# Kernel tuning notes

Hardware: AMD Instinct MI355X
Metric: run time of the kernel (lower is better)

The kernel has to match this reference:

```python
import jax, jax.numpy as jnp
import numpy as np

Lx, Ly, D, P = 4, 5, 4, 2
DEPTH = 5
TAU = 0.1
N = Lx * Ly
B = 64


def setup_inputs() -> dict:
    key = jax.random.key(0)
    k1, k2, k3 = jax.random.split(key, 3)
    # PEPS site tensors: [Lx, Ly, phys, up, down, left, right]; boundary bonds sliced to dim 1 at use.
    peps = jax.random.normal(k1, (Lx, Ly, P, D, D, D, D), dtype=jnp.float32) * 0.5
    # Two-site Trotter gate: expm(-tau * h) for a random symmetric two-body term h (4x4).
    h = jax.random.normal(k2, (4, 4), dtype=jnp.float32)
    h = 0.5 * (h + h.T)
    w, v = jnp.linalg.eigh(h)
    gate = (v * jnp.exp(-TAU * w)) @ v.T  # [4,4]
    x = jax.random.randint(k3, (B, N), 0, 2, dtype=jnp.int32)
    return {"x": x, "peps": peps, "gate": gate}


def _slice_boundary(site, i, j):
    # site: [p, u, d, l, r]; open boundary -> bond dim 1 on lattice edges
    if i == 0:
        site = site[:, :1]
    if i == Lx - 1:
        site = site[:, :, :1]
    if j == 0:
        site = site[:, :, :, :1]
    if j == Ly - 1:
        site = site[..., :1]
    return site


def _peps_statevector(peps):
    # Exact contraction of the open-boundary PEPS to the full 2^N statevector.
    rows = []
    for i in range(Lx):
        T = jnp.ones((1, 1, 1, 1), dtype=peps.dtype)  # [Pphys, Uup, Ddown, l]
        for j in range(Ly):
            s = _slice_boundary(peps[i, j], i, j)
            T = jnp.einsum('PUDl,pudlr->PpUuDdr', T, s)
            Pn, p, U, u, Dn, d, r = T.shape
            T = T.reshape(Pn * p, U * u, Dn * d, r)
        rows.append(T[..., 0])  # [2^Ly, up_bonds, down_bonds]
    S = jnp.ones((1, 1), dtype=peps.dtype)  # [Pphys, down_bonds]
    for row in rows:
        S = jnp.einsum('PU,QUD->PQD', S, row)
        a, b, c = S.shape
        S = S.reshape(a * b, c)
    return S[:, 0]  # [2^N]


def _apply_gate(psi, g, a, b):
    # g: [2,2,2,2] = gate[o1,o2,i1,i2]; psi: (2,)*N
    out = jnp.tensordot(g, psi, axes=([2, 3], [a, b]))
    return jnp.moveaxis(out, (0, 1), (a, b))


def _bonds():
    horiz = [((i, j), (i, j + 1)) for i in range(Lx) for j in range(Ly - 1)]
    vert = [((i, j), (i + 1, j)) for i in range(Lx - 1) for j in range(Ly)]
    return horiz + vert


def reference(x, peps, gate):
    psi = _peps_statevector(peps).reshape((2,) * N)
    g = gate.reshape(2, 2, 2, 2)
    bonds = _bonds()
    for _ in range(DEPTH):
        for (i1, j1), (i2, j2) in bonds:
            psi = _apply_gate(psi, g, i1 * Ly + j1, i2 * Ly + j2)
    psi = psi.reshape(-1)
    pw = 2 ** jnp.arange(N - 1, -1, -1, dtype=jnp.int32)
    idx = (x * pw).sum(axis=1)
    return psi[idx]  # [B] amplitudes
```

## Files before the change

### kernel.cpp

```cpp
#include <hip/hip_runtime.h>


#define PAD(i) ((i) + (((i) >> 4) << 2))
#define PIDX(i,j,p,u,d,l,r) (((((((i)*5+(j))*2+(p))*4+(u))*4+(d))*4+(l))*4+(r))

static constexpr int COL0  = 0;
static constexpr int COL1  = 4096;
static constexpr int COL2  = COL1 + 1048576;
static constexpr int COL3  = COL2 + 1048576;
static constexpr int COL4  = COL3 + 1048576;
static constexpr int M01TO = COL4 + 4096;
static constexpr int M34TO = M01TO + 65536;
static constexpr int T12TO = M34TO + 65536;
static constexpr int PSIO  = T12TO + 1048576;

__global__ __launch_bounds__(256) void k_build_cols(const float* __restrict__ peps,
                                                    float* __restrict__ ws) {
  __shared__ float p01[4096], p23[4096];
  int bid = blockIdx.x, t = threadIdx.x;
  if (bid < 384) {
    int col = 1 + (bid >> 7);
    int part = bid & 127;
#pragma unroll
    for (int k = 0; k < 16; ++k) {
      int e = k * 256 + t;
      int r12 = e & 15, l12 = (e >> 4) & 15, d2 = (e >> 8) & 3, p = e >> 10;
      int l1 = l12 >> 2, l2 = l12 & 3, r1 = r12 >> 2, r2 = r12 & 3;
      float s01 = 0.f, s23 = 0.f;
#pragma unroll
      for (int d = 0; d < 4; ++d) {
        s01 += peps[PIDX(0, col, (p >> 1), 0, d, l1, r1)] *
               peps[PIDX(1, col, (p & 1), d, d2, l2, r2)];
        s23 += peps[PIDX(2, col, (p >> 1), d2, d, l1, r1)] *
               peps[PIDX(3, col, (p & 1), d, 0, l2, r2)];
      }
      p01[e] = s01;
      p23[e] = s23;
    }
    __syncthreads();
    const int coloffs[3] = {COL1, COL2, COL3};
    float* out = ws + coloffs[col - 1];
#pragma unroll
    for (int k = 0; k < 8; ++k) {
      int eq = part * 8192 + (k * 256 + t) * 4;
      int r34b = eq & 15;
      int r12 = (eq >> 4) & 15, l34 = (eq >> 8) & 15, l12 = (eq >> 12) & 15;
      int p = eq >> 16;
      int pa = p >> 2, pb = p & 3;
      float4 acc = {0.f, 0.f, 0.f, 0.f};
#pragma unroll
      for (int d2 = 0; d2 < 4; ++d2) {
        float a01 = p01[((((pa * 4 + d2) << 4) | l12) << 4) | r12];
        const float4 b4 =
            *(const float4*)&p23[((((pb * 4 + d2) << 4) | l34) << 4) | r34b];
        acc.x += a01 * b4.x;
        acc.y += a01 * b4.y;
        acc.z += a01 * b4.z;
        acc.w += a01 * b4.w;
      }
      *(float4*)&out[eq] = acc;
    }
  } else {
    int col = (bid == 384) ? 0 : 4;
    const int lsh = (col == 0) ? 0 : 2;
    const int rsh = (col == 4) ? 0 : 2;
    const int ldim = 1 << lsh, rdim = 1 << rsh;
    const int LLB = 2 * lsh, RRB = 2 * rsh;
    const int LL = 1 << LLB, RR = 1 << RRB;
    int n12 = (LL * RR) << 4;
    for (int e = t; e < n12; e += 256) {
      int r12 = e & (RR - 1);
      int l12 = (e >> RRB) & (LL - 1);
      int d2 = (e >> (RRB + LLB)) & 3;
      int p = e >> (RRB + LLB + 2);
      int l1 = l12 >> lsh, l2 = l12 & (ldim - 1);
      int r1 = r12 >> rsh, r2 = r12 & (rdim - 1);
      float s01 = 0.f, s23 = 0.f;
      for (int d = 0; d < 4; ++d) {
        s01 += peps[PIDX(0, col, (p >> 1), 0, d, l1, r1)] *
               peps[PIDX(1, col, (p & 1), d, d2, l2, r2)];
        s23 += peps[PIDX(2, col, (p >> 1), d2, d, l1, r1)] *
               peps[PIDX(3, col, (p & 1), d, 0, l2, r2)];
      }
      p01[e] = s01;
      p23[e] = s23;
    }
    __syncthreads();
    const int LB = 2 * LLB, RB = 2 * RRB;
    int total = 16 << (LB + RB);
    float* out = ws + ((col == 0) ? COL0 : COL4);
    for (int e = t; e < total; e += 256) {
      int r = e & ((1 << RB) - 1);
      int l = (e >> RB) & ((1 << LB) - 1);
      int p = e >> (RB + LB);
      int r34 = r & (RR - 1), r12 = r >> RRB;
      int l34 = l & (LL - 1), l12 = l >> LLB;
      int pa = p >> 2, pb = p & 3;
      float s = 0.f;
      for (int d2 = 0; d2 < 4; ++d2) {
        s += p01[((((pa * 4 + d2) << LLB) | l12) << RRB) | r12] *
             p23[((((pb * 4 + d2) << LLB) | l34) << RRB) | r34];
      }
      out[e] = s;
    }
  }
}

__global__ __launch_bounds__(256) void k_small(const float* __restrict__ ws,
                                               float* __restrict__ m01,
                                               float* __restrict__ m34t) {
  __shared__ float c3buf[4112], c4buf[4112];
  int t = threadIdx.x;
  if (blockIdx.x < 64) {
    int c1 = blockIdx.x >> 2, q = blockIdx.x & 3;
    int r2l = t & 63, c0g = t >> 6;
    int R2 = q * 64 + r2l;
    const float* col0 = ws + COL0;
    const float* col1 = ws + COL1;
    float a0 = 0.f, a1 = 0.f, a2 = 0.f, a3 = 0.f;
    for (int R1 = 0; R1 < 256; ++R1) {
      float bv = col1[(c1 * 256 + R1) * 256 + R2];
      a0 += col0[(c0g * 4 + 0) * 256 + R1] * bv;
      a1 += col0[(c0g * 4 + 1) * 256 + R1] * bv;
      a2 += col0[(c0g * 4 + 2) * 256 + R1] * bv;
      a3 += col0[(c0g * 4 + 3) * 256 + R1] * bv;
    }
    m01[((c0g * 4 + 0) * 16 + c1) * 256 + R2] = a0;
    m01[((c0g * 4 + 1) * 16 + c1) * 256 + R2] = a1;
    m01[((c0g * 4 + 2) * 16 + c1) * 256 + R2] = a2;
    m01[((c0g * 4 + 3) * 16 + c1) * 256 + R2] = a3;
  } else {
    int L3 = blockIdx.x - 64;
    const float* col3 = ws + COL3;
    const float* col4 = ws + COL4;
    for (int e = t; e < 4096; e += 256) {
      c4buf[(e >> 8) * 257 + (e & 255)] = col4[e];
      c3buf[(e >> 8) * 257 + (e & 255)] =
          col3[(e >> 8) * 65536 + L3 * 256 + (e & 255)];
    }
    __syncthreads();
    int c3 = t >> 4, c4 = t & 15;
    float acc = 0.f;
    for (int B = 0; B < 256; ++B)
      acc += c3buf[c3 * 257 + B] * c4buf[c4 * 257 + B];
    m34t[L3 * 256 + t] = acc;
  }
}

__global__ __launch_bounds__(256) void k_t012(const float* __restrict__ m01,
                                              const float* __restrict__ col2,
                                              float* __restrict__ t012) {
  __shared__ float A[4096];
  int t = threadIdx.x;
  int c2 = blockIdx.x & 15, tg = blockIdx.x >> 4;
#pragma unroll
  for (int k = 0; k < 4; ++k)
    *(float4*)&A[(k * 256 + t) * 4] =
        *(const float4*)&m01[tg * 4096 + (k * 256 + t) * 4];
  __syncthreads();
  float acc[16] = {};
  for (int R2 = 0; R2 < 256; R2 += 4) {
    float b0 = col2[c2 * 65536 + (R2 + 0) * 256 + t];
    float b1 = col2[c2 * 65536 + (R2 + 1) * 256 + t];
    float b2 = col2[c2 * 65536 + (R2 + 2) * 256 + t];
    float b3 = col2[c2 * 65536 + (R2 + 3) * 256 + t];
#pragma unroll
    for (int i = 0; i < 16; ++i) {
      float4 a4 = *(const float4*)&A[i * 256 + R2];
      acc[i] += a4.x * b0 + a4.y * b1 + a4.z * b2 + a4.w * b3;
    }
  }
#pragma unroll
  for (int i = 0; i < 16; ++i)
    t012[c2 * 65536 + (tg * 16 + i) * 256 + t] = acc[i];
}

__global__ __launch_bounds__(256) void k_psi0(const float* __restrict__ t012,
                                              const float* __restrict__ m34t,
                                              float* __restrict__ psi) {
  __shared__ float A[4096];
  __shared__ float S[4112];
  int t = threadIdx.x;
  int tg = blockIdx.x;
#pragma unroll
  for (int i = 0; i < 16; ++i)
    A[i * 256 + t] = t012[i * 65536 + tg * 256 + t];
  __syncthreads();
  float acc[16] = {};
  for (int L3 = 0; L3 < 256; L3 += 4) {
    float b0 = m34t[(L3 + 0) * 256 + t];
    float b1 = m34t[(L3 + 1) * 256 + t];
    float b2 = m34t[(L3 + 2) * 256 + t];
    float b3 = m34t[(L3 + 3) * 256 + t];
#pragma unroll
    for (int i = 0; i < 16; ++i) {
      float4 a4 = *(const float4*)&A[i * 256 + L3];
      acc[i] += a4.x * b0 + a4.y * b1 + a4.z * b2 + a4.w * b3;
    }
  }
#pragma unroll
  for (int i = 0; i < 16; ++i) S[i * 257 + t] = acc[i];
  __syncthreads();
  int c3 = t >> 4, c2 = t & 15;
  int base = c3 * 65536 + (tg >> 4) * 256 + (tg & 15) * 16 + c2;
#pragma unroll
  for (int v = 0; v < 16; ++v)
    psi[base + v * 4096] = S[c2 * 257 + c3 * 16 + v];
}

template <int NB, int HI, int LO>
__device__ __forceinline__ void gate2(float* x, const float* __restrict__ g) {
  constexpr int H = 1 << HI, L = 1 << LO, N = 1 << NB;
#pragma unroll
  for (int o = 0; o < N; ++o) {
    if (o & (H | L)) continue;
    float v0 = x[o], v1 = x[o + L], v2 = x[o + H], v3 = x[o + H + L];
    x[o]         = g[0]  * v0 + g[1]  * v1 + g[2]  * v2 + g[3]  * v3;
    x[o + L]     = g[4]  * v0 + g[5]  * v1 + g[6]  * v2 + g[7]  * v3;
    x[o + H]     = g[8]  * v0 + g[9]  * v1 + g[10] * v2 + g[11] * v3;
    x[o + H + L] = g[12] * v0 + g[13] * v1 + g[14] * v2 + g[15] * v3;
  }
}

template <int ST>
__device__ __forceinline__ void vxf(float* s, const float* __restrict__ g, int b) {
  float x[16];
#pragma unroll
  for (int m = 0; m < 16; ++m) x[m] = s[PAD(b + m * ST)];
  gate2<4, 3, 2>(x, g);
  gate2<4, 2, 1>(x, g);
  gate2<4, 1, 0>(x, g);
#pragma unroll
  for (int m = 0; m < 16; ++m) s[PAD(b + m * ST)] = x[m];
}

template <int B2, int B1, int B0>
__device__ __forceinline__ void bondpair(float* s, const float* __restrict__ g,
                                         int t) {
  constexpr int MASK = (1 << B2) | (1 << B1) | (1 << B0);
  int b = 0, rem = t;
#pragma unroll
  for (int p = 0; p < 12; ++p) {
    if (!((MASK >> p) & 1)) {
      b |= (rem & 1) << p;
      rem >>= 1;
    }
  }
  float x[8];
#pragma unroll
  for (int m = 0; m < 8; ++m) {
    int off = ((m >> 2) & 1) * (1 << B2) + ((m >> 1) & 1) * (1 << B1) +
              (m & 1) * (1 << B0);
    x[m] = s[PAD(b + off)];
  }
  gate2<3, 2, 1>(x, g);
  gate2<3, 1, 0>(x, g);
#pragma unroll
  for (int m = 0; m < 8; ++m) {
    int off = ((m >> 2) & 1) * (1 << B2) + ((m >> 1) & 1) * (1 << B1) +
              (m & 1) * (1 << B0);
    s[PAD(b + off)] = x[m];
  }
}

__global__ __launch_bounds__(512) void k_P1(float* __restrict__ psi,
                                            const float* __restrict__ gate) {
  __shared__ float s[5120];
  float g[16];
#pragma unroll
  for (int i = 0; i < 16; ++i) g[i] = gate[i];
  int t = threadIdx.x;
  int o = blockIdx.x;
#pragma unroll
  for (int i = 0; i < 2; ++i) {
    int f = (i * 512 + t) * 4;
    *(float4*)(s + PAD(f)) = *(const float4*)(psi + o * 4096 + f);
  }
  __syncthreads();
  bondpair<8, 4, 0>(s, g, t);
  __syncthreads();
  bondpair<9, 5, 1>(s, g, t);
  __syncthreads();
  bondpair<10, 6, 2>(s, g, t);
  __syncthreads();
  bondpair<11, 7, 3>(s, g, t);
  __syncthreads();
  if (t < 256) vxf<256>(s, g, t);
  __syncthreads();
  if (t < 256) vxf<16>(s, g, ((t >> 4) << 8) | (t & 15));
  __syncthreads();
#pragma unroll
  for (int i = 0; i < 2; ++i) {
    int f = (i * 512 + t) * 4;
    *(float4*)(psi + o * 4096 + f) = *(const float4*)(s + PAD(f));
  }
}

template <bool LAST>
__global__ __launch_bounds__(512) void k_P2(float* __restrict__ psi,
                                            const float* __restrict__ gate,
                                            const int* __restrict__ x,
                                            float* __restrict__ out) {
  __shared__ float s[5120];
  float g[16];
#pragma unroll
  for (int i = 0; i < 16; ++i) g[i] = gate[i];
  int t = threadIdx.x;
  int o = blockIdx.x;
#pragma unroll
  for (int i = 0; i < 2; ++i) {
    int f = (i * 512 + t) * 4;
    int addr = (f >> 8) * 65536 + ((f >> 4) & 15) * 4096 + o * 16 + (f & 15);
    *(float4*)(s + PAD(f)) = *(const float4*)(psi + addr);
  }
  __syncthreads();
  bondpair<0, 8, 4>(s, g, t);
  __syncthreads();
  bondpair<1, 9, 5>(s, g, t);
  __syncthreads();
  bondpair<2, 10, 6>(s, g, t);
  __syncthreads();
  bondpair<3, 11, 7>(s, g, t);
  __syncthreads();
  if (t < 256) vxf<1>(s, g, t * 16);
  __syncthreads();
  if (t < 256) vxf<256>(s, g, t);
  __syncthreads();
  if (t < 256) vxf<16>(s, g, ((t >> 4) << 8) | (t & 15));
  __syncthreads();
  if (LAST) {
    if (t < 64) {
      int idx = 0;
#pragma unroll
      for (int q = 0; q < 20; ++q) {
        int i = q / 5, j = q % 5;
        int pos = (j == 0) ? (11 - i)
                 : (j == 1) ? (7 - i)
                 : (j == 2) ? (3 - i)
                 : (j == 3) ? (19 - i)
                            : (15 - i);
        idx |= x[t * 20 + q] << pos;
      }
      if (((idx >> 4) & 255) == o) {
        int local = ((idx >> 16) & 15) * 256 + ((idx >> 12) & 15) * 16 +
                    (idx & 15);
        out[t] = s[PAD(local)];
      }
    }
  } else {
#pragma unroll
    for (int i = 0; i < 2; ++i) {
      int f = (i * 512 + t) * 4;
      int addr = (f >> 8) * 65536 + ((f >> 4) & 15) * 4096 + o * 16 + (f & 15);
      *(float4*)(psi + addr) = *(const float4*)(s + PAD(f));
    }
  }
}

extern "C" void kernel_launch(void* const* d_in, const int* in_sizes, int n_in,
                              void* d_out, int out_size, void* d_ws, size_t ws_size,
                              hipStream_t stream) {
  const int* x = (const int*)d_in[0];
  const float* peps = (const float*)d_in[1];
  const float* gate = (const float*)d_in[2];
  float* ws = (float*)d_ws;
  float* psi = ws + PSIO;
  float* out = (float*)d_out;

  k_build_cols<<<386, 256, 0, stream>>>(peps, ws);
  k_small<<<320, 256, 0, stream>>>(ws, ws + M01TO, ws + M34TO);
  k_t012<<<256, 256, 0, stream>>>(ws + M01TO, ws + COL2, ws + T12TO);
  k_psi0<<<256, 256, 0, stream>>>(ws + T12TO, ws + M34TO, psi);

  for (int it = 0; it < 5; ++it) {
    k_P1<<<256, 512, 0, stream>>>(psi, gate);
    if (it < 4)
      k_P2<false><<<256, 512, 0, stream>>>(psi, gate, x, out);
    else
      k_P2<true><<<256, 512, 0, stream>>>(psi, gate, x, out);
  }
}
```

Measured before the change: 214.6 us.

## Remap gate passes to wave-local index sets, replacing block barriers with wave syncs

Reassigns the thread-to-amplitude mapping in the shared-memory gate passes so that consecutive bond-pair and vxf stages touch index subsets owned by a single wavefront. Several block-wide __syncthreads are replaced with a wave-local LDS wait plus wave barrier. This cuts block-level barrier stalls inside the per-tile gate sequence. Correctness depends on the new mappings keeping each dependent pair of stages inside one wave, and the new addressing may change LDS bank-conflict patterns.

```diff
diff --git a/kernel.cpp b/kernel.cpp
--- a/kernel.cpp
+++ b/kernel.cpp
@@ -3,6 +3,8 @@
 
 #define PAD(i) ((i) + (((i) >> 4) << 2))
 #define PIDX(i,j,p,u,d,l,r) (((((((i)*5+(j))*2+(p))*4+(u))*4+(d))*4+(l))*4+(r))
+#define WSYNC() do { asm volatile("s_waitcnt lgkmcnt(0)" ::: "memory"); \
+                     __builtin_amdgcn_wave_barrier(); } while (0)
 
 static constexpr int COL0  = 0;
 static constexpr int COL1  = 4096;
@@ -235,17 +237,8 @@
 }
 
 template <int B2, int B1, int B0>
-__device__ __forceinline__ void bondpair(float* s, const float* __restrict__ g,
-                                         int t) {
-  constexpr int MASK = (1 << B2) | (1 << B1) | (1 << B0);
-  int b = 0, rem = t;
-#pragma unroll
-  for (int p = 0; p < 12; ++p) {
-    if (!((MASK >> p) & 1)) {
-      b |= (rem & 1) << p;
-      rem >>= 1;
-    }
-  }
+__device__ __forceinline__ void bp_at(float* s, const float* __restrict__ g,
+                                      int b) {
   float x[8];
 #pragma unroll
   for (int m = 0; m < 8; ++m) {
@@ -263,6 +256,27 @@
   }
 }
 
+__device__ __forceinline__ int shA(int w, int l) {
+  return ((w >> 2) & 1) * 2048 + ((w >> 1) & 1) * 1024 + (w & 1) * 128 +
+         ((l >> 5) & 1) * 64 + ((l >> 4) & 1) * 8 + ((l >> 3) & 1) * 4;
+}
+__device__ __forceinline__ int shB(int w, int l) {
+  return ((w >> 2) & 1) * 512 + ((w >> 1) & 1) * 256 + (w & 1) * 32 +
+         ((l >> 5) & 1) * 16 + ((l >> 4) & 1) * 2 + ((l >> 3) & 1) * 1;
+}
+__device__ __forceinline__ int fb951(int l) {
+  return ((l >> 2) & 1) * 512 + ((l >> 1) & 1) * 32 + (l & 1) * 2;
+}
+__device__ __forceinline__ int fb840(int l) {
+  return ((l >> 2) & 1) * 256 + ((l >> 1) & 1) * 16 + (l & 1) * 1;
+}
+__device__ __forceinline__ int fb1173(int l) {
+  return ((l >> 2) & 1) * 2048 + ((l >> 1) & 1) * 128 + (l & 1) * 8;
+}
+__device__ __forceinline__ int fb1062(int l) {
+  return ((l >> 2) & 1) * 1024 + ((l >> 1) & 1) * 64 + (l & 1) * 4;
+}
+
 __global__ __launch_bounds__(512) void k_P1(float* __restrict__ psi,
                                             const float* __restrict__ gate) {
   __shared__ float s[5120];
@@ -271,23 +285,33 @@
   for (int i = 0; i < 16; ++i) g[i] = gate[i];
   int t = threadIdx.x;
   int o = blockIdx.x;
+  int w = t >> 6, l = t & 63;
 #pragma unroll
   for (int i = 0; i < 2; ++i) {
     int f = (i * 512 + t) * 4;
     *(float4*)(s + PAD(f)) = *(const float4*)(psi + o * 4096 + f);
   }
   __syncthreads();
-  bondpair<8, 4, 0>(s, g, t);
-  __syncthreads();
-  bondpair<9, 5, 1>(s, g, t);
-  __syncthreads();
-  bondpair<10, 6, 2>(s, g, t);
-  __syncthreads();
-  bondpair<11, 7, 3>(s, g, t);
-  __syncthreads();
-  if (t < 256) vxf<256>(s, g, t);
-  __syncthreads();
-  if (t < 256) vxf<16>(s, g, ((t >> 4) << 8) | (t & 15));
+  {
+    int sh = shA(w, l);
+    bp_at<8, 4, 0>(s, g, sh + fb951(l));
+    WSYNC();
+    bp_at<9, 5, 1>(s, g, sh + fb840(l));
+  }
+  __syncthreads();
+  {
+    int sh = shB(w, l);
+    bp_at<10, 6, 2>(s, g, sh + fb1173(l));
+    WSYNC();
+    bp_at<11, 7, 3>(s, g, sh + fb1062(l));
+  }
+  __syncthreads();
+  if (t < 256) {
+    int w2 = (t >> 6) & 3, l6 = t & 63;
+    vxf<256>(s, g, (l6 << 2) | w2);
+    WSYNC();
+    vxf<16>(s, g, (((l6 >> 2) & 15) << 8) | ((l6 & 3) << 2) | w2);
+  }
   __syncthreads();
 #pragma unroll
   for (int i = 0; i < 2; ++i) {
@@ -307,6 +331,7 @@
   for (int i = 0; i < 16; ++i) g[i] = gate[i];
   int t = threadIdx.x;
   int o = blockIdx.x;
+  int w = t >> 6, l = t & 63;
 #pragma unroll
   for (int i = 0; i < 2; ++i) {
     int f = (i * 512 + t) * 4;
@@ -314,17 +339,26 @@
     *(float4*)(s + PAD(f)) = *(const float4*)(psi + addr);
   }
   __syncthreads();
-  bondpair<0, 8, 4>(s, g, t);
-  __syncthreads();
-  bondpair<1, 9, 5>(s, g, t);
-  __syncthreads();
-  bondpair<2, 10, 6>(s, g, t);
-  __syncthreads();
-  bondpair<3, 11, 7>(s, g, t);
-  __syncthreads();
-  if (t < 256) vxf<1>(s, g, t * 16);
-  __syncthreads();
-  if (t < 256) vxf<256>(s, g, t);
+  {
+    int sh = shA(w, l);
+    bp_at<0, 8, 4>(s, g, sh + fb951(l));
+    WSYNC();
+    bp_at<1, 9, 5>(s, g, sh + fb840(l));
+  }
+  __syncthreads();
+  {
+    int sh = shB(w, l);
+    bp_at<2, 10, 6>(s, g, sh + fb1173(l));
+    WSYNC();
+    bp_at<3, 11, 7>(s, g, sh + fb1062(l));
+  }
+  __syncthreads();
+  if (t < 256) {
+    int w2 = (t >> 6) & 3, l6 = t & 63;
+    vxf<1>(s, g, (l6 << 6) | (w2 << 4));
+    WSYNC();
+    vxf<256>(s, g, (((l6 >> 4) & 3) << 6) | (w2 << 4) | (l6 & 15));
+  }
   __syncthreads();
   if (t < 256) vxf<16>(s, g, ((t >> 4) << 8) | (t & 15));
   __syncthreads();
```

Result: no change. 216.4 us (+0.8%).
